# Kernel tuning notes

Hardware: AMD Instinct MI355X
Metric: run time of the kernel (lower is better)

The kernel has to match this reference:

```python
import jax, jax.numpy as jnp
import numpy as np

NUM_EDGE_TYPES = 38
NUM_NODE_TYPES = 4
HIDDEN = 64
HOPS = 4
N_NODES = 100_000
N_EDGES = 1_600_000


def setup_inputs() -> dict:
    key = jax.random.key(0)
    ks = jax.random.split(key, 7)
    in_dim = NUM_EDGE_TYPES + 2 * NUM_NODE_TYPES  # 46
    return {
        "edge_index": jax.random.randint(ks[0], (2, N_EDGES), 0, N_NODES),
        "edge_type": jax.random.randint(ks[1], (N_EDGES,), 0, NUM_EDGE_TYPES),
        "node_type": jax.random.randint(ks[2], (N_NODES,), 0, NUM_NODE_TYPES),
        "W1": jax.random.normal(ks[3], (in_dim, HIDDEN), dtype=jnp.float32) * 0.1,
        "b1": jax.random.normal(ks[4], (HIDDEN,), dtype=jnp.float32) * 0.1,
        "W2": jax.random.normal(ks[5], (HIDDEN, 1), dtype=jnp.float32) * 0.1,
        "b2": jax.random.normal(ks[6], (1,), dtype=jnp.float32) * 0.1,
    }


def reference(edge_index, edge_type, node_type, W1, b1, W2, b2):
    src, dst = edge_index[0], edge_index[1]  # PyG: x_j = x[edge_index[0]], aggregate at edge_index[1]
    head_type = node_type[src]
    tail_type = node_type[dst]
    # Linear over concat of three one-hots == sum of three gathered weight rows + bias.
    h = (W1[edge_type]
         + W1[NUM_EDGE_TYPES + head_type]
         + W1[NUM_EDGE_TYPES + NUM_NODE_TYPES + tail_type]
         + b1)                                   # [E, HIDDEN]
    h = jax.nn.gelu(h)
    edge_emb = jax.nn.sigmoid(h @ W2 + b2)       # [E, 1]

    num_nodes = node_type.shape[0]
    aggr = jnp.zeros((num_nodes, 1), dtype=edge_emb.dtype)
    for _ in range(HOPS):
        msg = aggr[src] + edge_emb               # gather + add, [E, 1]
        aggr = jax.ops.segment_sum(msg, dst, num_segments=num_nodes)  # scatter-add
    return aggr
```

## Files before the change

kernel.cpp:

```cpp
#include <hip/hip_runtime.h>

#define NUM_EDGE_TYPES 38
#define NUM_NODE_TYPES 4
#define HIDDEN 64
#define TABLE_SIZE (NUM_EDGE_TYPES * NUM_NODE_TYPES * NUM_NODE_TYPES)
#define SRC_BITS 17
#define SRC_MASK ((1 << SRC_BITS) - 1)
#define BSHIFT 8
#define BNODES 256
#define MAXB 512
#define CHUNK 2048
#define PB 512
#define HB 1024
#define CAPC 6144

__device__ __forceinline__ float table_entry(int i, const float* __restrict__ W1,
                                             const float* __restrict__ b1,
                                             const float* __restrict__ W2,
                                             const float* __restrict__ b2) {
    int et = i >> 4, ht = (i >> 2) & 3, tt = i & 3;
    const float* r0 = W1 + et * HIDDEN;
    const float* r1 = W1 + (NUM_EDGE_TYPES + ht) * HIDDEN;
    const float* r2 = W1 + (NUM_EDGE_TYPES + NUM_NODE_TYPES + tt) * HIDDEN;
    float acc = b2[0];
#pragma unroll 8
    for (int k = 0; k < HIDDEN; ++k) {
        float h = r0[k] + r1[k] + r2[k] + b1[k];
        float u = 0.7978845608028654f * (h + 0.044715f * h * h * h);
        float g = 0.5f * h * (1.0f + tanhf(u));
        acc += g * W2[k];
    }
    return 1.0f / (1.0f + expf(-acc));
}

__global__ void table_kernel(const float* __restrict__ W1, const float* __restrict__ b1,
                             const float* __restrict__ W2, const float* __restrict__ b2,
                             float* __restrict__ table) {
    int i = blockIdx.x * blockDim.x + threadIdx.x;
    if (i < TABLE_SIZE) table[i] = table_entry(i, W1, b1, W2, b2);
}

__global__ void partition_kernel(const int* __restrict__ src, const int* __restrict__ dst,
                                 const int* __restrict__ etype, int* __restrict__ cursor,
                                 int* __restrict__ pack, int E, int nbk, int cap) {
    __shared__ int hist[MAXB];
    __shared__ int locCur[MAXB];
    for (int i = threadIdx.x; i < nbk; i += PB) hist[i] = 0;
    __syncthreads();
    int start = blockIdx.x * CHUNK;
    int end = min(start + CHUNK, E);
    if (end - start == CHUNK) {
        int j = start + threadIdx.x;
        int d[4], s[4], et[4], slot[4];
#pragma unroll
        for (int k = 0; k < 4; ++k) d[k] = dst[j + k * PB];
#pragma unroll
        for (int k = 0; k < 4; ++k) atomicAdd(&hist[d[k] >> BSHIFT], 1);
        __syncthreads();
        for (int i = threadIdx.x; i < nbk; i += PB) {
            int h = hist[i];
            locCur[i] = h ? i * cap + atomicAdd(&cursor[i], h) : 0;
        }
        __syncthreads();
#pragma unroll
        for (int k = 0; k < 4; ++k) s[k] = src[j + k * PB];
#pragma unroll
        for (int k = 0; k < 4; ++k) et[k] = etype[j + k * PB];
#pragma unroll
        for (int k = 0; k < 4; ++k) slot[k] = atomicAdd(&locCur[d[k] >> BSHIFT], 1);
#pragma unroll
        for (int k = 0; k < 4; ++k)
            pack[slot[k]] = (et[k] << (SRC_BITS + 8)) | ((d[k] & (BNODES - 1)) << SRC_BITS) | s[k];
    } else {
        for (int j = start + threadIdx.x; j < end; j += PB)
            atomicAdd(&hist[dst[j] >> BSHIFT], 1);
        __syncthreads();
        for (int i = threadIdx.x; i < nbk; i += PB) {
            int h = hist[i];
            locCur[i] = h ? i * cap + atomicAdd(&cursor[i], h) : 0;
        }
        __syncthreads();
        for (int j = start + threadIdx.x; j < end; j += PB) {
            int d = dst[j];
            int slot = atomicAdd(&locCur[d >> BSHIFT], 1);
            pack[slot] = (etype[j] << (SRC_BITS + 8)) | ((d & (BNODES - 1)) << SRC_BITS) | src[j];
        }
    }
}

__global__ void sort_base_kernel(int* __restrict__ pack, const int* __restrict__ cursor,
                                 const int* __restrict__ ntype, const float* __restrict__ table,
                                 float* __restrict__ base, int* __restrict__ nodeOffG,
                                 int N, int cap) {
    __shared__ int sortedL[CAPC];
    __shared__ float tbl[TABLE_SIZE];
    __shared__ int nodeCnt[BNODES];
    __shared__ int nodeOff[BNODES + 1];
    __shared__ unsigned char ntLoc[BNODES];
    int b = blockIdx.x;
    int node0 = b << BSHIFT;
    int tid = threadIdx.x;
    int st = b * cap;
    int c = min(cursor[b], cap);

    if (tid < TABLE_SIZE) tbl[tid] = table[tid];
    if (tid < BNODES) {
        nodeCnt[tid] = 0;
        int n = node0 + tid;
        ntLoc[tid] = (n < N) ? (unsigned char)ntype[n] : 0;
    }
    __syncthreads();

    for (int j = tid; j < c; j += HB)
        atomicAdd(&nodeCnt[(pack[st + j] >> SRC_BITS) & (BNODES - 1)], 1);
    __syncthreads();

    if (tid < 64) {
        int lane = tid;
        int v0 = nodeCnt[lane * 4], v1 = nodeCnt[lane * 4 + 1];
        int v2 = nodeCnt[lane * 4 + 2], v3 = nodeCnt[lane * 4 + 3];
        int s = v0 + v1 + v2 + v3;
        int inc = s;
        for (int d = 1; d < 64; d <<= 1) {
            int t = __shfl_up(inc, d, 64);
            if (lane >= d) inc += t;
        }
        int excl = inc - s;
        nodeOff[lane * 4]     = excl;
        nodeOff[lane * 4 + 1] = excl + v0;
        nodeOff[lane * 4 + 2] = excl + v0 + v1;
        nodeOff[lane * 4 + 3] = excl + v0 + v1 + v2;
        if (lane == 63) nodeOff[BNODES] = inc;
    }
    __syncthreads();
    if (tid < BNODES) nodeCnt[tid] = 0;
    __syncthreads();

    for (int j = tid; j < c; j += HB) {
        int p = pack[st + j];
        int dl = (p >> SRC_BITS) & (BNODES - 1);
        int r = atomicAdd(&nodeCnt[dl], 1);
        sortedL[nodeOff[dl] + r] = p;
    }
    __syncthreads();

    for (int j = tid; j < c; j += HB) pack[st + j] = sortedL[j];
    if (tid < BNODES) nodeOffG[(b << BSHIFT) + tid] = nodeOff[tid];

    int node = tid >> 2, l = tid & 3;
    int lo = nodeOff[node], hi = nodeOff[node + 1];
    int nt = ntLoc[node];
    float s = 0.0f;
    int j = lo + l;
    for (; j + 4 < hi; j += 8) {
        int p0 = sortedL[j], p1 = sortedL[j + 4];
        s += tbl[((((unsigned)p0) >> (SRC_BITS + 8)) << 4) | (ntype[p0 & SRC_MASK] << 2) | nt]
           + tbl[((((unsigned)p1) >> (SRC_BITS + 8)) << 4) | (ntype[p1 & SRC_MASK] << 2) | nt];
    }
    if (j < hi) {
        int p = sortedL[j];
        s += tbl[((((unsigned)p) >> (SRC_BITS + 8)) << 4) | (ntype[p & SRC_MASK] << 2) | nt];
    }
    s += __shfl_xor(s, 1, 64);
    s += __shfl_xor(s, 2, 64);
    int n = node0 + node;
    if (l == 0 && n < N) base[n] = s;
}

__global__ __launch_bounds__(512)
void hop_csr_kernel(const int* __restrict__ pack, const int* __restrict__ nodeOffG,
                    const int* __restrict__ cursor, const float* __restrict__ base,
                    const float* __restrict__ prev, float* __restrict__ out,
                    int N, int cap) {
    __shared__ int off[129];
    int blk = blockIdx.x;
    int b = blk >> 1;
    int half = blk & 1;
    int tid = threadIdx.x;
    int st = b * cap;
    int nodeBase = (b << BSHIFT) + half * 128;
    if (tid < 128) off[tid] = nodeOffG[(b << BSHIFT) + half * 128 + tid];
    else if (tid == 128)
        off[128] = half ? min(cursor[b], cap) : nodeOffG[(b << BSHIFT) + 128];
    __syncthreads();
    int node = tid >> 2, l = tid & 3;
    int lo = off[node], hi = off[node + 1];
    float s = 0.0f;
    int j = st + lo + l;
    int hiG = st + hi;
    for (; j + 4 < hiG; j += 8) {
        int p0 = pack[j], p1 = pack[j + 4];
        s += prev[p0 & SRC_MASK] + prev[p1 & SRC_MASK];
    }
    if (j < hiG) s += prev[pack[j] & SRC_MASK];
    s += __shfl_xor(s, 1, 64);
    s += __shfl_xor(s, 2, 64);
    int n = nodeBase + node;
    if (l == 0 && n < N) out[n] = base[n] + s;
}

__global__ void edge_base_kernel(const int* __restrict__ src, const int* __restrict__ dst,
                                 const int* __restrict__ etype, const int* __restrict__ ntype,
                                 const float* __restrict__ table, float* __restrict__ base, int E) {
    __shared__ float tbl[TABLE_SIZE];
    for (int i = threadIdx.x; i < TABLE_SIZE; i += blockDim.x) tbl[i] = table[i];
    __syncthreads();
    int e = blockIdx.x * blockDim.x + threadIdx.x;
    if (e >= E) return;
    int s = src[e];
    int d = dst[e];
    int idx = (etype[e] << 4) | (ntype[s] << 2) | ntype[d];
    atomicAdd(base + d, tbl[idx]);
}

__global__ void copy_kernel(const float* __restrict__ in, float* __restrict__ out, int N) {
    int i = blockIdx.x * blockDim.x + threadIdx.x;
    if (i < N) out[i] = in[i];
}

__global__ void edge_hop_kernel(const int* __restrict__ src, const int* __restrict__ dst,
                                const float* __restrict__ prev, float* __restrict__ next, int E) {
    int e = blockIdx.x * blockDim.x + threadIdx.x;
    if (e >= E) return;
    atomicAdd(next + dst[e], prev[src[e]]);
}

extern "C" void kernel_launch(void* const* d_in, const int* in_sizes, int n_in,
                              void* d_out, int out_size, void* d_ws, size_t ws_size,
                              hipStream_t stream) {
    const int* edge_index = (const int*)d_in[0];
    const int* etype      = (const int*)d_in[1];
    const int* ntype      = (const int*)d_in[2];
    const float* W1       = (const float*)d_in[3];
    const float* b1       = (const float*)d_in[4];
    const float* W2       = (const float*)d_in[5];
    const float* b2       = (const float*)d_in[6];

    const int E = in_sizes[1];
    const int N = in_sizes[2];
    const int* src = edge_index;
    const int* dst = edge_index + E;
    float* out = (float*)d_out;

    const int nbk = (N + BNODES - 1) >> BSHIFT;
    const int nChunks = (E + CHUNK - 1) / CHUNK;

    int cap = ((E / (nbk > 0 ? nbk : 1)) * 3 / 2 + 255) & ~255;
    if (cap < 512) cap = 512;
    size_t packElems = (size_t)nbk * cap;

    size_t need = (packElems + MAXB + (size_t)nbk * BNODES + 1024 + (size_t)3 * N) * 4 + 256;

    if (ws_size >= need && nbk <= MAXB && cap <= CAPC) {
        int* pack     = (int*)d_ws;
        int* cursor   = pack + packElems;
        int* nodeOffG = cursor + MAXB;
        float* table  = (float*)(nodeOffG + (size_t)nbk * BNODES);
        float* base   = table + 1024;
        float* bufA   = base + N;
        float* bufB   = bufA + N;

        hipMemsetAsync(cursor, 0, (size_t)nbk * sizeof(int), stream);
        table_kernel<<<(TABLE_SIZE + 255) / 256, 256, 0, stream>>>(W1, b1, W2, b2, table);
        partition_kernel<<<nChunks, PB, 0, stream>>>(src, dst, etype, cursor, pack, E, nbk, cap);
        sort_base_kernel<<<nbk, HB, 0, stream>>>(pack, cursor, ntype, table, base, nodeOffG, N, cap);
        hop_csr_kernel<<<2 * nbk, 512, 0, stream>>>(pack, nodeOffG, cursor, base, base, bufA, N, cap);
        hop_csr_kernel<<<2 * nbk, 512, 0, stream>>>(pack, nodeOffG, cursor, base, bufA, bufB, N, cap);
        hop_csr_kernel<<<2 * nbk, 512, 0, stream>>>(pack, nodeOffG, cursor, base, bufB, out, N, cap);
    } else {
        float* table = (float*)d_ws;
        float* base  = table + 1024;
        float* bufA  = base + N;
        float* bufB  = bufA + N;
        const int eb = (E + 255) / 256;
        const int nb = (N + 255) / 256;

        hipMemsetAsync(base, 0, (size_t)N * sizeof(float), stream);
        table_kernel<<<(TABLE_SIZE + 255) / 256, 256, 0, stream>>>(W1, b1, W2, b2, table);

        edge_base_kernel<<<eb, 256, 0, stream>>>(src, dst, etype, ntype, table, base, E);
        copy_kernel<<<nb, 256, 0, stream>>>(base, bufA, N);
        edge_hop_kernel<<<eb, 256, 0, stream>>>(src, dst, base, bufA, E);
        copy_kernel<<<nb, 256, 0, stream>>>(base, bufB, N);
        edge_hop_kernel<<<eb, 256, 0, stream>>>(src, dst, bufA, bufB, E);
        copy_kernel<<<nb, 256, 0, stream>>>(base, out, N);
        edge_hop_kernel<<<eb, 256, 0, stream>>>(src, dst, bufB, out, E);
    }
}
```

Measured before the change: 157.2 us.

## Vectorize partition and sort loads, stage bucket in LDS, fuse init, unroll hop gathers

Merges the cursor memset and table kernel into one init launch to save a launch. The partition kernel now reads four contiguous edges per thread with int4 loads instead of strided scalar loads. The sort kernel copies the bucket into a new LDS buffer with int4 loads, so global memory is read once instead of twice, and writes the sorted result back with int4 stores. The hop kernel unrolls its gather loop to four independent loads per iteration. The extra CAPC-int LDS array roughly doubles shared memory per sort block, which may lower occupancy, and the int4 accesses assume 16-byte alignment of pack offsets (cap is a multiple of 256, so this holds).

Result: faster. 150.0 us (-4.6%).

```diff
diff --git a/kernel.cpp b/kernel.cpp
--- a/kernel.cpp
+++ b/kernel.cpp
@@ -9,8 +9,8 @@
 #define BSHIFT 8
 #define BNODES 256
 #define MAXB 512
-#define CHUNK 2048
 #define PB 512
+#define CHUNK (PB * 4)
 #define HB 1024
 #define CAPC 6144
 
@@ -33,6 +33,14 @@
     return 1.0f / (1.0f + expf(-acc));
 }
 
+__global__ void init_kernel(const float* __restrict__ W1, const float* __restrict__ b1,
+                            const float* __restrict__ W2, const float* __restrict__ b2,
+                            float* __restrict__ table, int* __restrict__ cursor) {
+    int t = threadIdx.x;
+    if (t < MAXB) cursor[t] = 0;
+    if (t < TABLE_SIZE) table[t] = table_entry(t, W1, b1, W2, b2);
+}
+
 __global__ void table_kernel(const float* __restrict__ W1, const float* __restrict__ b1,
                              const float* __restrict__ W2, const float* __restrict__ b2,
                              float* __restrict__ table) {
@@ -50,27 +58,28 @@
     int start = blockIdx.x * CHUNK;
     int end = min(start + CHUNK, E);
     if (end - start == CHUNK) {
-        int j = start + threadIdx.x;
-        int d[4], s[4], et[4], slot[4];
-#pragma unroll
-        for (int k = 0; k < 4; ++k) d[k] = dst[j + k * PB];
-#pragma unroll
-        for (int k = 0; k < 4; ++k) atomicAdd(&hist[d[k] >> BSHIFT], 1);
+        int j = start + threadIdx.x * 4;
+        int4 d  = *(const int4*)(dst + j);
+        int4 s  = *(const int4*)(src + j);
+        int4 et = *(const int4*)(etype + j);
+        atomicAdd(&hist[d.x >> BSHIFT], 1);
+        atomicAdd(&hist[d.y >> BSHIFT], 1);
+        atomicAdd(&hist[d.z >> BSHIFT], 1);
+        atomicAdd(&hist[d.w >> BSHIFT], 1);
         __syncthreads();
         for (int i = threadIdx.x; i < nbk; i += PB) {
             int h = hist[i];
             locCur[i] = h ? i * cap + atomicAdd(&cursor[i], h) : 0;
         }
         __syncthreads();
-#pragma unroll
-        for (int k = 0; k < 4; ++k) s[k] = src[j + k * PB];
-#pragma unroll
-        for (int k = 0; k < 4; ++k) et[k] = etype[j + k * PB];
-#pragma unroll
-        for (int k = 0; k < 4; ++k) slot[k] = atomicAdd(&locCur[d[k] >> BSHIFT], 1);
-#pragma unroll
-        for (int k = 0; k < 4; ++k)
-            pack[slot[k]] = (et[k] << (SRC_BITS + 8)) | ((d[k] & (BNODES - 1)) << SRC_BITS) | s[k];
+        int t0 = atomicAdd(&locCur[d.x >> BSHIFT], 1);
+        int t1 = atomicAdd(&locCur[d.y >> BSHIFT], 1);
+        int t2 = atomicAdd(&locCur[d.z >> BSHIFT], 1);
+        int t3 = atomicAdd(&locCur[d.w >> BSHIFT], 1);
+        pack[t0] = (et.x << (SRC_BITS + 8)) | ((d.x & (BNODES - 1)) << SRC_BITS) | s.x;
+        pack[t1] = (et.y << (SRC_BITS + 8)) | ((d.y & (BNODES - 1)) << SRC_BITS) | s.y;
+        pack[t2] = (et.z << (SRC_BITS + 8)) | ((d.z & (BNODES - 1)) << SRC_BITS) | s.z;
+        pack[t3] = (et.w << (SRC_BITS + 8)) | ((d.w & (BNODES - 1)) << SRC_BITS) | s.w;
     } else {
         for (int j = start + threadIdx.x; j < end; j += PB)
             atomicAdd(&hist[dst[j] >> BSHIFT], 1);
@@ -92,6 +101,7 @@
                                  const int* __restrict__ ntype, const float* __restrict__ table,
                                  float* __restrict__ base, int* __restrict__ nodeOffG,
                                  int N, int cap) {
+    __shared__ int rawL[CAPC];
     __shared__ int sortedL[CAPC];
     __shared__ float tbl[TABLE_SIZE];
     __shared__ int nodeCnt[BNODES];
@@ -111,8 +121,20 @@
     }
     __syncthreads();
 
-    for (int j = tid; j < c; j += HB)
-        atomicAdd(&nodeCnt[(pack[st + j] >> SRC_BITS) & (BNODES - 1)], 1);
+    int c4 = c & ~3;
+    for (int j = tid * 4; j < c4; j += HB * 4) {
+        int4 v = *(const int4*)(pack + st + j);
+        *(int4*)(rawL + j) = v;
+        atomicAdd(&nodeCnt[(v.x >> SRC_BITS) & (BNODES - 1)], 1);
+        atomicAdd(&nodeCnt[(v.y >> SRC_BITS) & (BNODES - 1)], 1);
+        atomicAdd(&nodeCnt[(v.z >> SRC_BITS) & (BNODES - 1)], 1);
+        atomicAdd(&nodeCnt[(v.w >> SRC_BITS) & (BNODES - 1)], 1);
+    }
+    for (int j = c4 + tid; j < c; j += HB) {
+        int p = pack[st + j];
+        rawL[j] = p;
+        atomicAdd(&nodeCnt[(p >> SRC_BITS) & (BNODES - 1)], 1);
+    }
     __syncthreads();
 
     if (tid < 64) {
@@ -137,14 +159,16 @@
     __syncthreads();
 
     for (int j = tid; j < c; j += HB) {
-        int p = pack[st + j];
+        int p = rawL[j];
         int dl = (p >> SRC_BITS) & (BNODES - 1);
         int r = atomicAdd(&nodeCnt[dl], 1);
         sortedL[nodeOff[dl] + r] = p;
     }
     __syncthreads();
 
-    for (int j = tid; j < c; j += HB) pack[st + j] = sortedL[j];
+    for (int j = tid * 4; j < c4; j += HB * 4)
+        *(int4*)(pack + st + j) = *(const int4*)(sortedL + j);
+    for (int j = c4 + tid; j < c; j += HB) pack[st + j] = sortedL[j];
     if (tid < BNODES) nodeOffG[(b << BSHIFT) + tid] = nodeOff[tid];
 
     int node = tid >> 2, l = tid & 3;
@@ -188,11 +212,12 @@
     float s = 0.0f;
     int j = st + lo + l;
     int hiG = st + hi;
-    for (; j + 4 < hiG; j += 8) {
-        int p0 = pack[j], p1 = pack[j + 4];
-        s += prev[p0 & SRC_MASK] + prev[p1 & SRC_MASK];
-    }
-    if (j < hiG) s += prev[pack[j] & SRC_MASK];
+    for (; j + 12 < hiG; j += 16) {
+        int p0 = pack[j], p1 = pack[j + 4], p2 = pack[j + 8], p3 = pack[j + 12];
+        s += prev[p0 & SRC_MASK] + prev[p1 & SRC_MASK]
+           + prev[p2 & SRC_MASK] + prev[p3 & SRC_MASK];
+    }
+    for (; j < hiG; j += 4) s += prev[pack[j] & SRC_MASK];
     s += __shfl_xor(s, 1, 64);
     s += __shfl_xor(s, 2, 64);
     int n = nodeBase + node;
@@ -260,8 +285,7 @@
         float* bufA   = base + N;
         float* bufB   = bufA + N;
 
-        hipMemsetAsync(cursor, 0, (size_t)nbk * sizeof(int), stream);
-        table_kernel<<<(TABLE_SIZE + 255) / 256, 256, 0, stream>>>(W1, b1, W2, b2, table);
+        init_kernel<<<1, 1024, 0, stream>>>(W1, b1, W2, b2, table, cursor);
         partition_kernel<<<nChunks, PB, 0, stream>>>(src, dst, etype, cursor, pack, E, nbk, cap);
         sort_base_kernel<<<nbk, HB, 0, stream>>>(pack, cursor, ntype, table, base, nodeOffG, N, cap);
         hop_csr_kernel<<<2 * nbk, 512, 0, stream>>>(pack, nodeOffG, cursor, base, base, bufA, N, cap);
```
